# Optimization experiments

Hardware: AMD Instinct MI355X
Metric: run time of the kernel (lower is better)

## Reference

```python
import jax, jax.numpy as jnp
from jax import lax
import numpy as np

G, K = 8, 9  # deformable groups, 3x3 kernel taps


def conv1x1_bn_relu(x, W, scale, bias):
    # Conv2d 1x1 (no bias) + folded eval-mode BatchNorm (per-channel scale/bias) + ReLU
    y = jnp.einsum('bchw,oc->bohw', x, W)
    return jax.nn.relu(y * scale[None, :, None, None] + bias[None, :, None, None])


def dcn_v2(feat, offset_feat, W_om, b_om, W_dcn, b_dcn):
    # Modulated deformable conv v2, 3x3, stride 1, pad 1, dilation 1,
    # deformable_groups=G, extra_offset_mask: offsets/mask predicted from offset_feat.
    B, C, H, W_ = feat.shape
    Cg = C // G
    om = lax.conv_general_dilated(offset_feat, W_om, (1, 1), ((1, 1), (1, 1)))
    om = om + b_om[None, :, None, None]              # [B, 3*G*K, H, W]
    o1, o2, m = jnp.split(om, 3, axis=1)
    off_y = o1.reshape(B, G, K, H, W_)
    off_x = o2.reshape(B, G, K, H, W_)
    mask = jax.nn.sigmoid(m).reshape(B, G, K, H, W_)
    dk = jnp.arange(3) - 1
    dkh = jnp.repeat(dk, 3)   # tap row offset,  k = kh*3 + kw
    dkw = jnp.tile(dk, 3)     # tap col offset
    hh = jnp.arange(H, dtype=feat.dtype)
    ww = jnp.arange(W_, dtype=feat.dtype)
    py = hh[None, None, None, :, None] + dkh[None, None, :, None, None].astype(feat.dtype) + off_y
    px = ww[None, None, None, None, :] + dkw[None, None, :, None, None].astype(feat.dtype) + off_x
    y0 = jnp.floor(py); x0 = jnp.floor(px)
    ty = py - y0; tx = px - x0
    xg = feat.reshape(B, G, Cg, H * W_)

    def gather(idx):  # idx [B,G,K,H,W] int32 -> [B,G,Cg,K,H,W]
        f = lambda xf, i: xf[:, i]
        return jax.vmap(jax.vmap(f))(xg, idx)

    val = jnp.zeros((B, G, Cg, K, H, W_), dtype=feat.dtype)
    y0i = y0.astype(jnp.int32); x0i = x0.astype(jnp.int32)
    for dy, wy in ((0, 1.0 - ty), (1, ty)):
        iy = y0i + dy
        vy = (iy >= 0) & (iy < H)
        iyc = jnp.clip(iy, 0, H - 1)
        for dx, wx in ((0, 1.0 - tx), (1, tx)):
            ix = x0i + dx
            v = vy & (ix >= 0) & (ix < W_)
            idx = iyc * W_ + jnp.clip(ix, 0, W_ - 1)
            w = (wy * wx) * v.astype(feat.dtype)      # zero-padding outside
            val = val + w[:, :, None] * gather(idx)
    val = val * mask[:, :, None]                      # modulation
    Wd = W_dcn.reshape(W_dcn.shape[0], G, Cg, K)      # [Cout, G, Cg, K]
    out = jnp.einsum('bgckhw,ogck->bohw', val, Wd) + b_dcn[None, :, None, None]
    return out


def setup_inputs() -> dict:
    key = jax.random.key(0)
    ks = jax.random.split(key, 16)
    B, C, H, W_ = 8, 128, 64, 64
    Cd = C // 2  # dcn out channels = 64
    d = {}
    d['feat_l'] = jax.random.normal(ks[0], (B, C, H, W_), jnp.float32)
    d['feat_s'] = jax.random.normal(ks[1], (B, C, H // 2, W_ // 2), jnp.float32)
    d['W_fsm'] = jax.random.normal(ks[2], (C, C), jnp.float32) / np.sqrt(C)
    d['s_fsm'] = 1.0 + 0.1 * jax.random.normal(ks[3], (C,), jnp.float32)
    d['b_fsm'] = 0.1 * jax.random.normal(ks[4], (C,), jnp.float32)
    d['W_off'] = jax.random.normal(ks[5], (C, 2 * C), jnp.float32) / np.sqrt(2 * C)
    d['s_off'] = 1.0 + 0.1 * jax.random.normal(ks[6], (C,), jnp.float32)
    d['b_off'] = 0.1 * jax.random.normal(ks[7], (C,), jnp.float32)
    d['W_om'] = 0.05 * jax.random.normal(ks[8], (3 * G * K, C, 3, 3), jnp.float32)
    d['b_om'] = jnp.zeros((3 * G * K,), jnp.float32)
    d['W_dcn'] = jax.random.normal(ks[9], (Cd, C, 3, 3), jnp.float32) / np.sqrt(C * 9)
    d['b_dcn'] = 0.1 * jax.random.normal(ks[10], (Cd,), jnp.float32)
    d['W_cat'] = jax.random.normal(ks[11], (C, Cd), jnp.float32) / np.sqrt(Cd)
    d['s_cat'] = 1.0 + 0.1 * jax.random.normal(ks[12], (C,), jnp.float32)
    d['b_cat'] = 0.1 * jax.random.normal(ks[13], (C,), jnp.float32)
    return d


def reference(feat_l, feat_s, W_fsm, s_fsm, b_fsm, W_off, s_off, b_off,
              W_om, b_om, W_dcn, b_dcn, W_cat, s_cat, b_cat):
    # nearest upsample x2 (F.interpolate nearest to feat_l spatial size)
    feat_up = jnp.repeat(jnp.repeat(feat_s, 2, axis=2), 2, axis=3)
    feat_arm = conv1x1_bn_relu(feat_l, W_fsm, s_fsm, b_fsm)
    offset = conv1x1_bn_relu(jnp.concatenate([feat_arm, feat_up * 2.0], axis=1),
                             W_off, s_off, b_off)
    feat_align = jax.nn.relu(dcn_v2(feat_up, offset, W_om, b_om, W_dcn, b_dcn))
    feat = conv1x1_bn_relu(feat_align, W_cat, s_cat, b_cat) + feat_arm
    return (feat, feat_arm)
```

## Files before the change

### kernel.cpp

```cpp
#include <hip/hip_runtime.h>


typedef __attribute__((ext_vector_type(8))) short short8;
typedef __attribute__((ext_vector_type(4))) float f32x4;
typedef _Float16 __attribute__((ext_vector_type(2))) h2;

static __device__ __forceinline__ unsigned short f2bf(float x) {
    union { float f; unsigned int u; } v; v.f = x;
    return (unsigned short)((v.u + 0x7FFF + ((v.u >> 16) & 1)) >> 16);
}
static __device__ __forceinline__ unsigned short f2h(float x) {
    union { _Float16 h; unsigned short u; } v; v.h = (_Float16)x;
    return v.u;
}

__global__ __launch_bounds__(256) void k_prep(const float* __restrict__ fs,
        uint4* __restrict__ fsT4, uint4* __restrict__ fsC4,
        const float* __restrict__ W_fsm, const float* __restrict__ W_off,
        const float* __restrict__ W_cat, const float* __restrict__ W_dcn,
        const float* __restrict__ W_om,
        unsigned short* __restrict__ wbfsm, unsigned short* __restrict__ wboff,
        unsigned short* __restrict__ wbcat, unsigned short* __restrict__ wbdcn,
        unsigned short* __restrict__ wb2) {
    __shared__ unsigned short st[64 * 136];
    const int t = threadIdx.x;
    if (blockIdx.x < 128) {
        unsigned int* st32 = (unsigned int*)st;
        const int b = blockIdx.x >> 4;
        const int p0 = (blockIdx.x & 15) << 6;
        for (int i = t; i < 64 * 64; i += 256) {
            int c2 = i >> 6, px = i & 63;
            float v0 = fs[(((b << 7) + 2 * c2) << 10) + p0 + px];
            float v1 = fs[(((b << 7) + 2 * c2 + 1) << 10) + p0 + px];
            st32[px * 68 + c2] = (unsigned int)f2bf(v0) | ((unsigned int)f2bf(v1) << 16);
        }
        __syncthreads();
        for (int i = t; i < 64 * 16; i += 256) {
            int px = i >> 4, q = i & 15;
            fsT4[(((b << 10) + p0 + px) << 4) + q] = ((const uint4*)(st + px * 136))[q];
        }
        __syncthreads();
        for (int i = t; i < 64 * 64; i += 256) {
            int c2 = i >> 6, px = i & 63;
            float v0 = fs[(((b << 7) + 2 * c2) << 10) + p0 + px];
            float v1 = fs[(((b << 7) + 2 * c2 + 1) << 10) + p0 + px];
            st32[px * 68 + c2] = (unsigned int)f2h(v0) | ((unsigned int)f2h(v1) << 16);
        }
        __syncthreads();
        for (int i = t; i < 64 * 16; i += 256) {
            int ci = i >> 6, px = i & 63;
            fsC4[(b << 14) + (ci << 10) + p0 + px] = ((const uint4*)(st + px * 136))[ci];
        }
        return;
    }
    int idx = (blockIdx.x - 128) * 256 + t;
    int lane = idx & 63;
    int ml = lane & 15, kl = (lane >> 4) * 8;
    unsigned short tmp[8];
    if (idx < 2048) {
        int r = idx >> 6;
        int o = (r % 8) * 16 + ml, k0 = (r / 8) * 32 + kl;
#pragma unroll
        for (int j = 0; j < 8; j++) tmp[j] = f2bf(W_fsm[o * 128 + k0 + j]);
        ((uint4*)wbfsm)[idx] = *(const uint4*)tmp;
    } else if (idx < 6144) {
        int i2 = idx - 2048;
        int r = i2 >> 6;
        int o = (r % 8) * 16 + ml, k0 = (r / 8) * 32 + kl;
#pragma unroll
        for (int j = 0; j < 8; j++) {
            int k = k0 + j;
            float f = W_off[o * 256 + k];
            if (k >= 128) f *= 2.0f;
            tmp[j] = f2bf(f);
        }
        ((uint4*)wboff)[i2] = *(const uint4*)tmp;
    } else if (idx < 7168) {
        int i2 = idx - 6144;
        int r = i2 >> 6;
        int o = (r % 8) * 16 + ml, k0 = (r / 8) * 32 + kl;
#pragma unroll
        for (int j = 0; j < 8; j++) tmp[j] = f2bf(W_cat[o * 64 + k0 + j]);
        ((uint4*)wbcat)[i2] = *(const uint4*)tmp;
    } else if (idx < 16384) {
        int i2 = idx - 7168;
        int r = i2 >> 6;
        int o = (r & 3) * 16 + ml, k0 = (r >> 2) * 32 + kl;
#pragma unroll
        for (int j = 0; j < 8; j++) {
            int k = k0 + j;
            int g = k / 144;
            int rem = k - g * 144;
            tmp[j] = f2h(W_dcn[(o * 128 + g * 16 + (rem & 15)) * 9 + (rem >> 4)]);
        }
        ((uint4*)wbdcn)[i2] = *(const uint4*)tmp;
    } else if (idx < 48640) {
        int i2 = idx - 16384;
        int r = i2 >> 6;
        int nt = r % 14, kk = r / 14;
        int tap = kk >> 2, cc = kk & 3;
        int o = nt * 16 + ml;
        int c0 = cc * 32 + kl;
#pragma unroll
        for (int j = 0; j < 8; j++) {
            float v = (o < 216) ? W_om[(o * 128 + (c0 + j)) * 9 + tap] : 0.0f;
            tmp[j] = f2bf(v);
        }
        ((uint4*)wb2)[i2] = *(const uint4*)tmp;
    }
}

__global__ __launch_bounds__(512, 6) void k12(const float* __restrict__ feat_l,
        const uint4* __restrict__ fsT4,
        const unsigned short* __restrict__ wbf, const unsigned short* __restrict__ wbo,
        const float* __restrict__ s_fsm, const float* __restrict__ b_fsm,
        const float* __restrict__ s_off, const float* __restrict__ b_off,
        float* __restrict__ feat_arm, unsigned short* __restrict__ offT) {
    __shared__ unsigned short A1[64 * 136];
    __shared__ unsigned short A2[64 * 264];
    const int t = threadIdx.x;
    const int b = blockIdx.x >> 6;
    const int h = blockIdx.x & 63;
    const int hw0 = h << 6;
    unsigned int* A1w = (unsigned int*)A1;
    for (int i = t; i < 64 * 64; i += 512) {
        int c2 = i >> 6, px = i & 63;
        float v0 = feat_l[(((b << 7) + 2 * c2) << 12) + hw0 + px];
        float v1 = feat_l[(((b << 7) + 2 * c2 + 1) << 12) + hw0 + px];
        A1w[px * 68 + c2] = (unsigned int)f2bf(v0) | ((unsigned int)f2bf(v1) << 16);
    }
    {
        const int h2 = h >> 1;
        int px2 = t >> 4, q = t & 15;
        uint4 v = fsT4[(((b << 10) + (h2 << 5) + px2) << 4) + q];
        ((uint4*)(A2 + (2 * px2) * 264 + 128))[q] = v;
        ((uint4*)(A2 + (2 * px2 + 1) * 264 + 128))[q] = v;
    }
    __syncthreads();
    const int lane = t & 63;
    const int w = __builtin_amdgcn_readfirstlane(t >> 6);
    const int ph = w & 1;
    const int nq4 = w >> 1;
    const int m = lane & 15, ko = lane >> 4;
    f32x4 acc[2][2];
#pragma unroll
    for (int i = 0; i < 2; i++)
#pragma unroll
        for (int j = 0; j < 2; j++) acc[i][j] = (f32x4){0.f, 0.f, 0.f, 0.f};
#pragma unroll
    for (int kk = 0; kk < 4; kk++) {
        short8 a8[2];
#pragma unroll
        for (int mt = 0; mt < 2; mt++)
            a8[mt] = *(const short8*)(A1 + ((ph << 5) + (mt << 4) + m) * 136 + kk * 32 + ko * 8);
#pragma unroll
        for (int nt2 = 0; nt2 < 2; nt2++) {
            uint4 bu = ((const uint4*)wbf)[((kk << 3) + (nq4 << 1) + nt2) * 64 + lane];
#pragma unroll
            for (int mt = 0; mt < 2; mt++)
                acc[mt][nt2] = __builtin_amdgcn_mfma_f32_16x16x32_bf16(
                    a8[mt], *(short8*)&bu, acc[mt][nt2], 0, 0, 0);
        }
    }
#pragma unroll
    for (int nt2 = 0; nt2 < 2; nt2++) {
        int o = (((nq4 << 1) + nt2) << 4) + m;
        float sc = s_fsm[o], bi = b_fsm[o];
#pragma unroll
        for (int mt = 0; mt < 2; mt++) {
            int px0 = (ph << 5) + (mt << 4) + (ko << 2);
            f32x4 v;
#pragma unroll
            for (int r = 0; r < 4; r++) {
                float vv = fmaf(acc[mt][nt2][r], sc, bi);
                vv = vv > 0.f ? vv : 0.f;
                v[r] = vv;
                A2[(px0 + r) * 264 + o] = f2bf(vv);
            }
            *(f32x4*)(feat_arm + ((((b << 7) + o) << 12) + hw0 + px0)) = v;
        }
    }
    __syncthreads();
    f32x4 acc2[2][2];
#pragma unroll
    for (int i = 0; i < 2; i++)
#pragma unroll
        for (int j = 0; j < 2; j++) acc2[i][j] = (f32x4){0.f, 0.f, 0.f, 0.f};
#pragma unroll
    for (int kk = 0; kk < 8; kk++) {
        short8 a8[2];
#pragma unroll
        for (int mt = 0; mt < 2; mt++)
            a8[mt] = *(const short8*)(A2 + ((ph << 5) + (mt << 4) + m) * 264 + kk * 32 + ko * 8);
#pragma unroll
        for (int nt2 = 0; nt2 < 2; nt2++) {
            uint4 bu = ((const uint4*)wbo)[((kk << 3) + (nq4 << 1) + nt2) * 64 + lane];
#pragma unroll
            for (int mt = 0; mt < 2; mt++)
                acc2[mt][nt2] = __builtin_amdgcn_mfma_f32_16x16x32_bf16(
                    a8[mt], *(short8*)&bu, acc2[mt][nt2], 0, 0, 0);
        }
    }
    __syncthreads();
#pragma unroll
    for (int nt2 = 0; nt2 < 2; nt2++) {
        int o = (((nq4 << 1) + nt2) << 4) + m;
        float sc = s_off[o], bi = b_off[o];
#pragma unroll
        for (int mt = 0; mt < 2; mt++) {
            int px0 = (ph << 5) + (mt << 4) + (ko << 2);
#pragma unroll
            for (int r = 0; r < 4; r++) {
                float v = fmaf(acc2[mt][nt2][r], sc, bi);
                v = v > 0.f ? v : 0.f;
                A2[(px0 + r) * 264 + o] = f2bf(v);
            }
        }
    }
    __syncthreads();
    for (int i = t; i < 64 * 16; i += 512) {
        int px = i >> 4, q = i & 15;
        ((uint4*)offT)[(((b << 12) + hw0 + px) << 4) + q] = ((const uint4*)(A2 + px * 264))[q];
    }
}

static __device__ __forceinline__ void dcn_prep(int kk, int ko, const float* omrow,
        float fh, float fw, const uint4* __restrict__ fsC4, int b14,
        uint4& c00, uint4& c01, uint4& c10, uint4& c11,
        float& w00, float& w01, float& w10, float& w11) {
    int k0 = (kk << 5) + (ko << 3);
    int g = k0 / 144;
    int rem = k0 - g * 144;
    int tap = rem >> 4;
    int c0 = rem & 15;
    int ch = g * 9 + tap;
    float oy = omrow[ch];
    float ox = omrow[72 + ch];
    float mmv = omrow[144 + ch];
    float py = fh + (float)(tap / 3 - 1) + oy;
    float pxx = fw + (float)(tap % 3 - 1) + ox;
    float y0f = floorf(py), x0f = floorf(pxx);
    float tyf = py - y0f, txf = pxx - x0f;
    int y0i = (int)y0f, x0i = (int)x0f;
    int y1i = y0i + 1, x1i = x0i + 1;
    bool vy0 = (y0i >= 0) && (y0i < 64);
    bool vy1 = (y1i >= 0) && (y1i < 64);
    bool vx0 = (x0i >= 0) && (x0i < 64);
    bool vx1 = (x1i >= 0) && (x1i < 64);
    w00 = (vy0 && vx0) ? (1.0f - tyf) * (1.0f - txf) * mmv : 0.0f;
    w01 = (vy0 && vx1) ? (1.0f - tyf) * txf * mmv : 0.0f;
    w10 = (vy1 && vx0) ? tyf * (1.0f - txf) * mmv : 0.0f;
    w11 = (vy1 && vx1) ? tyf * txf * mmv : 0.0f;
    int yc0 = y0i < 0 ? 0 : (y0i > 63 ? 63 : y0i);
    int yc1 = y1i < 0 ? 0 : (y1i > 63 ? 63 : y1i);
    int xc0 = x0i < 0 ? 0 : (x0i > 63 ? 63 : x0i);
    int xc1 = x1i < 0 ? 0 : (x1i > 63 ? 63 : x1i);
    int row0 = (yc0 >> 1) << 5, row1 = (yc1 >> 1) << 5;
    int ci = g * 2 + (c0 >> 3);
    const uint4* base = fsC4 + b14 + (ci << 10);
    c00 = base[row0 + (xc0 >> 1)];
    c01 = base[row0 + (xc1 >> 1)];
    c10 = base[row1 + (xc0 >> 1)];
    c11 = base[row1 + (xc1 >> 1)];
}

static __device__ __forceinline__ void dcn_consume(int kk,
        const uint4& c00, const uint4& c01, const uint4& c10, const uint4& c11,
        float w00, float w01, float w10, float w11,
        const uint4* __restrict__ wbd4, int lane, f32x4* accd) {
    _Float16 h00 = (_Float16)w00, h01 = (_Float16)w01;
    _Float16 h10 = (_Float16)w10, h11 = (_Float16)w11;
    h2 W00 = (h2){h00, h00}, W01 = (h2){h01, h01};
    h2 W10 = (h2){h10, h10}, W11 = (h2){h11, h11};
    union { uint4 u; h2 h[4]; } U00, U01, U10, U11;
    U00.u = c00; U01.u = c01; U10.u = c10; U11.u = c11;
    union { short8 s; h2 h[4]; } av;
#pragma unroll
    for (int c = 0; c < 4; c++)
        av.h[c] = U00.h[c] * W00 + U01.h[c] * W01 + U10.h[c] * W10 + U11.h[c] * W11;
    const uint4* wb = wbd4 + (kk << 2) * 64 + lane;
    __builtin_amdgcn_s_setprio(1);
#pragma unroll
    for (int nt = 0; nt < 4; nt++) {
        uint4 bu = wb[nt * 64];
        accd[nt] = __builtin_amdgcn_mfma_f32_16x16x32_f16(av.s, *(short8*)&bu, accd[nt], 0, 0, 0);
    }
    __builtin_amdgcn_s_setprio(0);
}

__global__ __launch_bounds__(512, 4) void k_omdcn(
        const unsigned short* __restrict__ offT, const uint4* __restrict__ fsC4,
        const unsigned short* __restrict__ Wb2, const float* __restrict__ bom,
        const unsigned short* __restrict__ wbd, const float* __restrict__ bd,
        const unsigned short* __restrict__ wbc,
        const float* __restrict__ s_cat, const float* __restrict__ b_cat,
        const float* __restrict__ feat_arm, float* __restrict__ feat) {
    __shared__ float LDSf[16384];
    unsigned short* st = (unsigned short*)LDSf;
    float* omT = LDSf;
    float* Rbuf = LDSf;
    unsigned short* A3 = (unsigned short*)(LDSf + 13888);
    const uint4* offT4 = (const uint4*)offT;
    const uint4* W4 = (const uint4*)Wb2;
    const uint4* wbd4 = (const uint4*)wbd;
    const int t = threadIdx.x;
    const int b = blockIdx.x >> 6;
    const int h = blockIdx.x & 63;
    for (int i = t; i < 3 * 66 * 16; i += 512) {
        int q = i & 15;
        int rp = i >> 4;
        int r = rp / 66, p = rp - r * 66;
        int gy = h + r - 1, gx = p - 1;
        uint4 v = make_uint4(0, 0, 0, 0);
        if (gy >= 0 && gy < 64 && gx >= 0 && gx < 64)
            v = offT4[((((b << 6) + gy) << 6) + gx) * 16 + q];
        ((uint4*)(st + rp * 136))[q] = v;
    }
    __syncthreads();
    const int lane = t & 63;
    const int w = __builtin_amdgcn_readfirstlane(t >> 6);
    const int m = lane & 15, ko = lane >> 4;
    f32x4 acc[2][4];
#pragma unroll
    for (int i = 0; i < 2; i++)
#pragma unroll
        for (int j = 0; j < 4; j++) acc[i][j] = (f32x4){0.f, 0.f, 0.f, 0.f};
    if (w < 7) {
        const int ntb = w << 1;
        uint4 b4c[2];
#pragma unroll
        for (int nt2 = 0; nt2 < 2; nt2++)
            b4c[nt2] = W4[((ntb + nt2) << 6) + lane];
#pragma unroll
        for (int kk = 0; kk < 36; kk++) {
            const int tap = kk >> 2, cc = kk & 3;
            const int dy = tap / 3, dx = tap - dy * 3;
            uint4 b4n[2];
            if (kk < 35) {
#pragma unroll
                for (int nt2 = 0; nt2 < 2; nt2++)
                    b4n[nt2] = W4[(((kk + 1) * 14 + ntb + nt2) << 6) + lane];
            }
            short8 a8[4];
#pragma unroll
            for (int mt = 0; mt < 4; mt++) {
                int p = mt * 16 + m + dx;
                a8[mt] = *(const short8*)(st + (dy * 66 + p) * 136 + (cc << 5) + (ko << 3));
            }
            __builtin_amdgcn_s_setprio(1);
#pragma unroll
            for (int nt2 = 0; nt2 < 2; nt2++)
#pragma unroll
                for (int mt = 0; mt < 4; mt++)
                    acc[nt2][mt] = __builtin_amdgcn_mfma_f32_16x16x32_bf16(
                        a8[mt], *(short8*)&b4c[nt2], acc[nt2][mt], 0, 0, 0);
            __builtin_amdgcn_s_setprio(0);
            if (kk < 35) {
#pragma unroll
                for (int nt2 = 0; nt2 < 2; nt2++) b4c[nt2] = b4n[nt2];
            }
        }
    }
    __syncthreads();
    if (w < 7) {
#pragma unroll
        for (int nt2 = 0; nt2 < 2; nt2++) {
            int o = (((w << 1) + nt2) << 4) + m;
            if (o < 216) {
                float bv = bom[o];
                bool ismask = (o >= 144);
#pragma unroll
                for (int mt = 0; mt < 4; mt++) {
                    f32x4 v = acc[nt2][mt];
#pragma unroll
                    for (int r = 0; r < 4; r++) {
                        float val = v[r] + bv;
                        if (ismask) val = 1.0f / (1.0f + __expf(-val));
                        omT[(mt * 16 + (ko << 2) + r) * 217 + o] = val;
                    }
                }
            }
        }
    }
    __syncthreads();
    const int nq = w & 3;
    const int kh = w >> 2;
    const int px = (nq << 4) + m;
    const float fh = (float)h, fw = (float)px;
    const int b14 = b << 14;
    const float* omrow = omT + px * 217;
    f32x4 accd[4];
#pragma unroll
    for (int nt = 0; nt < 4; nt++) accd[nt] = (f32x4){0.f, 0.f, 0.f, 0.f};
    {
        const int dk0 = kh * 18;
        uint4 s00[3], s01[3], s10[3], s11[3];
        float t00[3], t01[3], t10[3], t11[3];
#pragma unroll
        for (int i = 0; i < 2; i++)
            dcn_prep(dk0 + i, ko, omrow, fh, fw, fsC4, b14,
                     s00[i], s01[i], s10[i], s11[i], t00[i], t01[i], t10[i], t11[i]);
#pragma unroll
        for (int kki = 0; kki < 18; kki++) {
            const int sc_ = kki % 3;
            if (kki < 16) {
                const int sp = (kki + 2) % 3;
                dcn_prep(dk0 + kki + 2, ko, omrow, fh, fw, fsC4, b14,
                         s00[sp], s01[sp], s10[sp], s11[sp],
                         t00[sp], t01[sp], t10[sp], t11[sp]);
            }
            dcn_consume(dk0 + kki, s00[sc_], s01[sc_], s10[sc_], s11[sc_],
                        t00[sc_], t01[sc_], t10[sc_], t11[sc_], wbd4, lane, accd);
        }
    }
    __syncthreads();
    if (kh == 1) {
#pragma unroll
        for (int nt = 0; nt < 4; nt++)
            *(f32x4*)(Rbuf + ((nq << 6) + lane) * 20 + (nt << 2)) = accd[nt];
    }
    __syncthreads();
    if (kh == 0) {
#pragma unroll
        for (int nt = 0; nt < 4; nt++)
            accd[nt] += *(const f32x4*)(Rbuf + ((nq << 6) + lane) * 20 + (nt << 2));
#pragma unroll
        for (int nt = 0; nt < 4; nt++) {
            int o = (nt << 4) + m;
            float bv = bd[o];
#pragma unroll
            for (int r = 0; r < 4; r++) {
                float v = accd[nt][r] + bv;
                v = v > 0.f ? v : 0.f;
                A3[((nq << 4) + (ko << 2) + r) * 72 + o] = f2bf(v);
            }
        }
    }
    __syncthreads();
    f32x4 acc2[4];
#pragma unroll
    for (int nt2 = 0; nt2 < 4; nt2++) acc2[nt2] = (f32x4){0.f, 0.f, 0.f, 0.f};
#pragma unroll
    for (int kk2 = 0; kk2 < 2; kk2++) {
        short8 av = *(const short8*)(A3 + ((nq << 4) + m) * 72 + kk2 * 32 + (ko << 3));
#pragma unroll
        for (int nt2 = 0; nt2 < 4; nt2++) {
            uint4 bu = ((const uint4*)wbc)[(kk2 * 8 + (kh << 2) + nt2) * 64 + lane];
            acc2[nt2] = __builtin_amdgcn_mfma_f32_16x16x32_bf16(av, *(short8*)&bu, acc2[nt2], 0, 0, 0);
        }
    }
    {
        const int px0 = (nq << 4) + (ko << 2);
        const int base = (b << 19) + (h << 6) + px0;
        f32x4 fa[4];
#pragma unroll
        for (int nt2 = 0; nt2 < 4; nt2++) {
            int o = (((kh << 2) + nt2) << 4) + m;
            fa[nt2] = *(const f32x4*)(feat_arm + base + (o << 12));
        }
#pragma unroll
        for (int nt2 = 0; nt2 < 4; nt2++) {
            int o = (((kh << 2) + nt2) << 4) + m;
            float sc = s_cat[o], bi = b_cat[o];
            f32x4 v;
#pragma unroll
            for (int r = 0; r < 4; r++) {
                float vv = fmaf(acc2[nt2][r], sc, bi);
                vv = vv > 0.f ? vv : 0.f;
                v[r] = vv + fa[nt2][r];
            }
            *(f32x4*)(feat + base + (o << 12)) = v;
        }
    }
}

extern "C" void kernel_launch(void* const* d_in, const int* in_sizes, int n_in,
                              void* d_out, int out_size, void* d_ws, size_t ws_size,
                              hipStream_t stream) {
    const float* feat_l = (const float*)d_in[0];
    const float* feat_s = (const float*)d_in[1];
    const float* W_fsm  = (const float*)d_in[2];
    const float* s_fsm  = (const float*)d_in[3];
    const float* b_fsm  = (const float*)d_in[4];
    const float* W_off  = (const float*)d_in[5];
    const float* s_off  = (const float*)d_in[6];
    const float* b_off  = (const float*)d_in[7];
    const float* W_om   = (const float*)d_in[8];
    const float* b_om   = (const float*)d_in[9];
    const float* W_dcn  = (const float*)d_in[10];
    const float* b_dcn  = (const float*)d_in[11];
    const float* W_cat  = (const float*)d_in[12];
    const float* s_cat  = (const float*)d_in[13];
    const float* b_cat  = (const float*)d_in[14];

    float* feat     = (float*)d_out;
    float* feat_arm = feat + 4194304;

    float* ws = (float*)d_ws;
    unsigned short* offT = (unsigned short*)ws;
    uint4* fsT4  = (uint4*)(ws + 9175040);
    unsigned short* wb2   = (unsigned short*)(ws + 9699328);
    unsigned short* wbfsm = (unsigned short*)(ws + 9846784);
    unsigned short* wboff = (unsigned short*)(ws + 9854976);
    unsigned short* wbcat = (unsigned short*)(ws + 9871360);
    unsigned short* wbdcn = (unsigned short*)(ws + 9875456);
    uint4* fsC4  = (uint4*)(ws + 9912320);

    k_prep<<<318, 256, 0, stream>>>(feat_s, fsT4, fsC4, W_fsm, W_off, W_cat,
                                    W_dcn, W_om, wbfsm, wboff, wbcat, wbdcn, wb2);

    k12<<<512, 512, 0, stream>>>(feat_l, fsT4, wbfsm, wboff,
                                 s_fsm, b_fsm, s_off, b_off, feat_arm, offT);
    k_omdcn<<<512, 512, 0, stream>>>(offT, fsC4, wb2, b_om, wbdcn, b_dcn,
                                     wbcat, s_cat, b_cat, feat_arm, feat);
}
```

Measured before the change: 158.1 us.

## Switch DCN GEMM to 32x32x16 MFMA with 4-way K split and tree reduction

The deformable-conv GEMM now uses 32x32x16 f16 MFMA tiles instead of 16x16x32. Each wave covers 32 pixels and one quarter of the K dimension (two groups, 18 sampling steps) instead of 16 pixels and half of K. The DCN weight prep layout is reordered to match the new operand format. The software-pipelined prefetch of bilinear samples is removed, and partial sums are combined through a two-level LDS reduction with extra barriers. This aims to cut redundant bilinear sampling per MFMA and raise MFMA efficiency, at the cost of more accumulator registers, less explicit latency hiding, and more synchronisation.

Measured after the change: 160.9 us. No clear change (+1.8%).

```diff
diff --git a/kernel.cpp b/kernel.cpp
--- a/kernel.cpp
+++ b/kernel.cpp
@@ -3,7 +3,10 @@
 
 typedef __attribute__((ext_vector_type(8))) short short8;
 typedef __attribute__((ext_vector_type(4))) float f32x4;
+typedef __attribute__((ext_vector_type(16))) float f32x16;
 typedef _Float16 __attribute__((ext_vector_type(2))) h2;
+
+union F16u { f32x16 v; f32x4 q[4]; };
 
 static __device__ __forceinline__ unsigned short f2bf(float x) {
     union { float f; unsigned int u; } v; v.f = x;
@@ -85,7 +88,8 @@
     } else if (idx < 16384) {
         int i2 = idx - 7168;
         int r = i2 >> 6;
-        int o = (r & 3) * 16 + ml, k0 = (r >> 2) * 32 + kl;
+        int o = (r & 1) * 32 + (lane & 31);
+        int k0 = (r >> 1) * 16 + (lane >> 5) * 8;
 #pragma unroll
         for (int j = 0; j < 8; j++) {
             int k = k0 + j;
@@ -222,70 +226,6 @@
         int px = i >> 4, q = i & 15;
         ((uint4*)offT)[(((b << 12) + hw0 + px) << 4) + q] = ((const uint4*)(A2 + px * 264))[q];
     }
-}
-
-static __device__ __forceinline__ void dcn_prep(int kk, int ko, const float* omrow,
-        float fh, float fw, const uint4* __restrict__ fsC4, int b14,
-        uint4& c00, uint4& c01, uint4& c10, uint4& c11,
-        float& w00, float& w01, float& w10, float& w11) {
-    int k0 = (kk << 5) + (ko << 3);
-    int g = k0 / 144;
-    int rem = k0 - g * 144;
-    int tap = rem >> 4;
-    int c0 = rem & 15;
-    int ch = g * 9 + tap;
-    float oy = omrow[ch];
-    float ox = omrow[72 + ch];
-    float mmv = omrow[144 + ch];
-    float py = fh + (float)(tap / 3 - 1) + oy;
-    float pxx = fw + (float)(tap % 3 - 1) + ox;
-    float y0f = floorf(py), x0f = floorf(pxx);
-    float tyf = py - y0f, txf = pxx - x0f;
-    int y0i = (int)y0f, x0i = (int)x0f;
-    int y1i = y0i + 1, x1i = x0i + 1;
-    bool vy0 = (y0i >= 0) && (y0i < 64);
-    bool vy1 = (y1i >= 0) && (y1i < 64);
-    bool vx0 = (x0i >= 0) && (x0i < 64);
-    bool vx1 = (x1i >= 0) && (x1i < 64);
-    w00 = (vy0 && vx0) ? (1.0f - tyf) * (1.0f - txf) * mmv : 0.0f;
-    w01 = (vy0 && vx1) ? (1.0f - tyf) * txf * mmv : 0.0f;
-    w10 = (vy1 && vx0) ? tyf * (1.0f - txf) * mmv : 0.0f;
-    w11 = (vy1 && vx1) ? tyf * txf * mmv : 0.0f;
-    int yc0 = y0i < 0 ? 0 : (y0i > 63 ? 63 : y0i);
-    int yc1 = y1i < 0 ? 0 : (y1i > 63 ? 63 : y1i);
-    int xc0 = x0i < 0 ? 0 : (x0i > 63 ? 63 : x0i);
-    int xc1 = x1i < 0 ? 0 : (x1i > 63 ? 63 : x1i);
-    int row0 = (yc0 >> 1) << 5, row1 = (yc1 >> 1) << 5;
-    int ci = g * 2 + (c0 >> 3);
-    const uint4* base = fsC4 + b14 + (ci << 10);
-    c00 = base[row0 + (xc0 >> 1)];
-    c01 = base[row0 + (xc1 >> 1)];
-    c10 = base[row1 + (xc0 >> 1)];
-    c11 = base[row1 + (xc1 >> 1)];
-}
-
-static __device__ __forceinline__ void dcn_consume(int kk,
-        const uint4& c00, const uint4& c01, const uint4& c10, const uint4& c11,
-        float w00, float w01, float w10, float w11,
-        const uint4* __restrict__ wbd4, int lane, f32x4* accd) {
-    _Float16 h00 = (_Float16)w00, h01 = (_Float16)w01;
-    _Float16 h10 = (_Float16)w10, h11 = (_Float16)w11;
-    h2 W00 = (h2){h00, h00}, W01 = (h2){h01, h01};
-    h2 W10 = (h2){h10, h10}, W11 = (h2){h11, h11};
-    union { uint4 u; h2 h[4]; } U00, U01, U10, U11;
-    U00.u = c00; U01.u = c01; U10.u = c10; U11.u = c11;
-    union { short8 s; h2 h[4]; } av;
-#pragma unroll
-    for (int c = 0; c < 4; c++)
-        av.h[c] = U00.h[c] * W00 + U01.h[c] * W01 + U10.h[c] * W10 + U11.h[c] * W11;
-    const uint4* wb = wbd4 + (kk << 2) * 64 + lane;
-    __builtin_amdgcn_s_setprio(1);
-#pragma unroll
-    for (int nt = 0; nt < 4; nt++) {
-        uint4 bu = wb[nt * 64];
-        accd[nt] = __builtin_amdgcn_mfma_f32_16x16x32_f16(av.s, *(short8*)&bu, accd[nt], 0, 0, 0);
-    }
-    __builtin_amdgcn_s_setprio(0);
 }
 
 __global__ __launch_bounds__(512, 4) void k_omdcn(
@@ -383,60 +323,120 @@
         }
     }
     __syncthreads();
+    const int p2 = w & 1;
+    const int kq = w >> 1;
+    const int oct = lane >> 5;
+    const int l31 = lane & 31;
+    const int px = (p2 << 5) + l31;
+    const float fh = (float)h, fw = (float)px;
+    const int b14 = b << 14;
+    const float* omrow = omT + px * 217 + kq * 18;
+    const uint4* bp0 = fsC4 + b14 + (((kq << 2) + oct) << 10);
+    const uint4* wbbase = wbd4 + (kq * 36) * 64 + lane;
+    F16u acc3[2];
+#pragma unroll
+    for (int nt = 0; nt < 2; nt++)
+#pragma unroll
+        for (int q = 0; q < 4; q++) acc3[nt].q[q] = (f32x4){0.f, 0.f, 0.f, 0.f};
+#pragma unroll
+    for (int si = 0; si < 18; si++) {
+        const int tap = si % 9;
+        const int dy = tap / 3, dx = tap - dy * 3;
+        float oy = omrow[si];
+        float ox = omrow[72 + si];
+        float mmv = omrow[144 + si];
+        float py = fh + (float)(dy - 1) + oy;
+        float pxx = fw + (float)(dx - 1) + ox;
+        float y0f = floorf(py), x0f = floorf(pxx);
+        float tyf = py - y0f, txf = pxx - x0f;
+        int y0i = (int)y0f, x0i = (int)x0f;
+        int y1i = y0i + 1, x1i = x0i + 1;
+        bool vy0 = (y0i >= 0) && (y0i < 64);
+        bool vy1 = (y1i >= 0) && (y1i < 64);
+        bool vx0 = (x0i >= 0) && (x0i < 64);
+        bool vx1 = (x1i >= 0) && (x1i < 64);
+        float w00 = (vy0 && vx0) ? (1.0f - tyf) * (1.0f - txf) * mmv : 0.0f;
+        float w01 = (vy0 && vx1) ? (1.0f - tyf) * txf * mmv : 0.0f;
+        float w10 = (vy1 && vx0) ? tyf * (1.0f - txf) * mmv : 0.0f;
+        float w11 = (vy1 && vx1) ? tyf * txf * mmv : 0.0f;
+        int yc0 = y0i < 0 ? 0 : (y0i > 63 ? 63 : y0i);
+        int yc1 = y1i < 0 ? 0 : (y1i > 63 ? 63 : y1i);
+        int xc0 = x0i < 0 ? 0 : (x0i > 63 ? 63 : x0i);
+        int xc1 = x1i < 0 ? 0 : (x1i > 63 ? 63 : x1i);
+        int row0 = (yc0 >> 1) << 5, row1 = (yc1 >> 1) << 5;
+        const uint4* bpp = (si < 9) ? bp0 : (bp0 + 2048);
+        uint4 c00 = bpp[row0 + (xc0 >> 1)];
+        uint4 c01 = bpp[row0 + (xc1 >> 1)];
+        uint4 c10 = bpp[row1 + (xc0 >> 1)];
+        uint4 c11 = bpp[row1 + (xc1 >> 1)];
+        _Float16 h00 = (_Float16)w00, h01 = (_Float16)w01;
+        _Float16 h10 = (_Float16)w10, h11 = (_Float16)w11;
+        h2 W00 = (h2){h00, h00}, W01 = (h2){h01, h01};
+        h2 W10 = (h2){h10, h10}, W11 = (h2){h11, h11};
+        union { uint4 u; h2 h[4]; } U00, U01, U10, U11;
+        U00.u = c00; U01.u = c01; U10.u = c10; U11.u = c11;
+        union { short8 s; h2 h[4]; } av;
+#pragma unroll
+        for (int c = 0; c < 4; c++)
+            av.h[c] = U00.h[c] * W00 + U01.h[c] * W01 + U10.h[c] * W10 + U11.h[c] * W11;
+        uint4 bu0 = wbbase[(si * 2) * 64];
+        uint4 bu1 = wbbase[(si * 2 + 1) * 64];
+        __builtin_amdgcn_s_setprio(1);
+        acc3[0].v = __builtin_amdgcn_mfma_f32_32x32x16_f16(av.s, *(short8*)&bu0, acc3[0].v, 0, 0, 0);
+        acc3[1].v = __builtin_amdgcn_mfma_f32_32x32x16_f16(av.s, *(short8*)&bu1, acc3[1].v, 0, 0, 0);
+        __builtin_amdgcn_s_setprio(0);
+    }
+    __syncthreads();
+    if (kq >= 2) {
+        float* rb = Rbuf + ((((kq - 2) << 1) + p2) * 64 + lane) * 32;
+#pragma unroll
+        for (int nt = 0; nt < 2; nt++)
+#pragma unroll
+            for (int q = 0; q < 4; q++)
+                *(f32x4*)(rb + (nt << 4) + (q << 2)) = acc3[nt].q[q];
+    }
+    __syncthreads();
+    if (kq < 2) {
+        const float* rb = Rbuf + (((kq << 1) + p2) * 64 + lane) * 32;
+#pragma unroll
+        for (int nt = 0; nt < 2; nt++)
+#pragma unroll
+            for (int q = 0; q < 4; q++)
+                acc3[nt].q[q] += *(const f32x4*)(rb + (nt << 4) + (q << 2));
+    }
+    __syncthreads();
+    if (kq == 1) {
+        float* rb = Rbuf + (p2 * 64 + lane) * 32;
+#pragma unroll
+        for (int nt = 0; nt < 2; nt++)
+#pragma unroll
+            for (int q = 0; q < 4; q++)
+                *(f32x4*)(rb + (nt << 4) + (q << 2)) = acc3[nt].q[q];
+    }
+    __syncthreads();
+    if (kq == 0) {
+        const float* rb = Rbuf + (p2 * 64 + lane) * 32;
+#pragma unroll
+        for (int nt = 0; nt < 2; nt++)
+#pragma unroll
+            for (int q = 0; q < 4; q++)
+                acc3[nt].q[q] += *(const f32x4*)(rb + (nt << 4) + (q << 2));
+#pragma unroll
+        for (int nt = 0; nt < 2; nt++) {
+            int o = (nt << 5) + l31;
+            float bv = bd[o];
+#pragma unroll
+            for (int r = 0; r < 16; r++) {
+                int rowm = (r & 3) + ((r >> 2) << 3) + (oct << 2);
+                float v = acc3[nt].v[r] + bv;
+                v = v > 0.f ? v : 0.f;
+                A3[((p2 << 5) + rowm) * 72 + o] = f2bf(v);
+            }
+        }
+    }
+    __syncthreads();
     const int nq = w & 3;
     const int kh = w >> 2;
-    const int px = (nq << 4) + m;
-    const float fh = (float)h, fw = (float)px;
-    const int b14 = b << 14;
-    const float* omrow = omT + px * 217;
-    f32x4 accd[4];
-#pragma unroll
-    for (int nt = 0; nt < 4; nt++) accd[nt] = (f32x4){0.f, 0.f, 0.f, 0.f};
-    {
-        const int dk0 = kh * 18;
-        uint4 s00[3], s01[3], s10[3], s11[3];
-        float t00[3], t01[3], t10[3], t11[3];
-#pragma unroll
-        for (int i = 0; i < 2; i++)
-            dcn_prep(dk0 + i, ko, omrow, fh, fw, fsC4, b14,
-                     s00[i], s01[i], s10[i], s11[i], t00[i], t01[i], t10[i], t11[i]);
-#pragma unroll
-        for (int kki = 0; kki < 18; kki++) {
-            const int sc_ = kki % 3;
-            if (kki < 16) {
-                const int sp = (kki + 2) % 3;
-                dcn_prep(dk0 + kki + 2, ko, omrow, fh, fw, fsC4, b14,
-                         s00[sp], s01[sp], s10[sp], s11[sp],
-                         t00[sp], t01[sp], t10[sp], t11[sp]);
-            }
-            dcn_consume(dk0 + kki, s00[sc_], s01[sc_], s10[sc_], s11[sc_],
-                        t00[sc_], t01[sc_], t10[sc_], t11[sc_], wbd4, lane, accd);
-        }
-    }
-    __syncthreads();
-    if (kh == 1) {
-#pragma unroll
-        for (int nt = 0; nt < 4; nt++)
-            *(f32x4*)(Rbuf + ((nq << 6) + lane) * 20 + (nt << 2)) = accd[nt];
-    }
-    __syncthreads();
-    if (kh == 0) {
-#pragma unroll
-        for (int nt = 0; nt < 4; nt++)
-            accd[nt] += *(const f32x4*)(Rbuf + ((nq << 6) + lane) * 20 + (nt << 2));
-#pragma unroll
-        for (int nt = 0; nt < 4; nt++) {
-            int o = (nt << 4) + m;
-            float bv = bd[o];
-#pragma unroll
-            for (int r = 0; r < 4; r++) {
-                float v = accd[nt][r] + bv;
-                v = v > 0.f ? v : 0.f;
-                A3[((nq << 4) + (ko << 2) + r) * 72 + o] = f2bf(v);
-            }
-        }
-    }
-    __syncthreads();
     f32x4 acc2[4];
 #pragma unroll
     for (int nt2 = 0; nt2 < 4; nt2++) acc2[nt2] = (f32x4){0.f, 0.f, 0.f, 0.f};
```
